# Kernel tuning notes

Measured on AMD Instinct MI355X. Metric: run time of the kernel, lower is better.

Reference implementation:

```python
import jax, jax.numpy as jnp
import numpy as np

N_VAR = 524288   # code.n
DV = 3           # regular variable-node degree
DC = 6           # regular check-node degree
N_CHK = N_VAR * DV // DC
T = 10           # max_iterations


def setup_inputs() -> dict:
    key = jax.random.key(0)
    k1, k2, k3 = jax.random.split(key, 3)
    rng = np.random.default_rng(0)
    # Regular (3,6) Tanner graph via random socket permutation (edge list == H sparsity)
    edge_var = np.repeat(np.arange(N_VAR, dtype=np.int32), DV)
    edge_chk = rng.permutation(np.repeat(np.arange(N_CHK, dtype=np.int32), DC)).astype(np.int32)
    llr = jax.random.normal(k1, (N_VAR,), jnp.float32) * 2.0
    beta = jax.random.normal(k2, (T,), jnp.float32) * 0.1   # per-iteration dc-shared offsets
    alpha = jax.random.normal(k3, (T,), jnp.float32) * 0.1  # per-iteration dv-shared offsets
    return {"llr": llr, "beta": beta, "alpha": alpha,
            "edge_var": jnp.asarray(edge_var), "edge_chk": jnp.asarray(edge_chk),
            "n_checks": N_CHK}


def reference(llr, beta, alpha, edge_var, edge_chk, n_checks):
    E = edge_var.shape[0]
    n = llr.shape[0]
    e_idx = jnp.arange(E)

    def step(carry, ba):
        v2c, _ = carry
        b, a = ba
        mags = jnp.abs(v2c)
        sgn = jnp.sign(v2c)
        # per-check min / argmin(first) / second-min over incoming edge magnitudes
        min1 = jax.ops.segment_min(mags, edge_chk, num_segments=n_checks)
        amin = jax.ops.segment_min(jnp.where(mags == min1[edge_chk], e_idx, E),
                                   edge_chk, num_segments=n_checks)
        is_amin = e_idx == amin[edge_chk]
        min2 = jax.ops.segment_min(jnp.where(is_amin, jnp.inf, mags),
                                   edge_chk, num_segments=n_checks)
        min2 = jnp.where(jnp.isinf(min2), min1, min2)  # degree-1 checks: min2 = min1
        raw = jnp.where(is_amin, min2[edge_chk], min1[edge_chk])
        # product of signs excluding self (signs are +-1)
        sprod = jax.ops.segment_prod(sgn, edge_chk, num_segments=n_checks)
        c2v = sprod[edge_chk] * sgn * (jax.nn.relu(raw - b) - a)
        # variable node: extrinsic sum
        tot = jax.ops.segment_sum(c2v, edge_var, num_segments=n)
        v2c_new = llr[edge_var] + tot[edge_var] - c2v
        return (v2c_new, c2v), None

    v2c0 = llr[edge_var]
    (v2c_f, c2v_f), _ = jax.lax.scan(step, (v2c0, jnp.zeros_like(v2c0)), (beta, alpha))
    posterior = llr + jax.ops.segment_sum(c2v_f, edge_var, num_segments=n)
    decoded_bits = (posterior < 0).astype(jnp.int32)
    return decoded_bits, posterior
```

## Files before the change

### kernel.cpp

```cpp
#include <hip/hip_runtime.h>
#include <math.h>

#define DC_C 6
#define NRANGE 8
#define VCH 2048


__device__ __forceinline__ float c2v_from_rec(uint3 r, int j) {
    float val = ((r.z >> j) & 1u) ? __uint_as_float(r.x) : __uint_as_float(r.y);
    float s = ((r.z >> (16 + j)) & 1u) ? 0.0f
            : (((r.z >> (8 + j)) & 1u) ? -1.0f : 1.0f);
    return s * val;
}

__global__ void build_a(const int* __restrict__ edge_chk,
                        unsigned int* __restrict__ cnt8,
                        unsigned long long* __restrict__ pos64,
                        int n) {
    int v = blockIdx.x * blockDim.x + threadIdx.x;
    if (v >= n) return;
    int c0 = edge_chk[v * 3 + 0];
    int c1 = edge_chk[v * 3 + 1];
    int c2 = edge_chk[v * 3 + 2];
    unsigned int sh0 = (c0 & 7) * 4, sh1 = (c1 & 7) * 4, sh2 = (c2 & 7) * 4;
    unsigned int o0 = atomicAdd(&cnt8[c0 >> 3], 1u << sh0);
    unsigned int o1 = atomicAdd(&cnt8[c1 >> 3], 1u << sh1);
    unsigned int o2 = atomicAdd(&cnt8[c2 >> 3], 1u << sh2);
    int j0 = (o0 >> sh0) & 0xF;
    int j1 = (o1 >> sh1) & 0xF;
    int j2 = (o2 >> sh2) & 0xF;
    unsigned long long s0 = (unsigned long long)(c0 * DC_C + j0);
    unsigned long long s1 = (unsigned long long)(c1 * DC_C + j1);
    unsigned long long s2 = (unsigned long long)(c2 * DC_C + j2);
    pos64[v] = s0 | (s1 << 21) | (s2 << 42);
}

__global__ void build_b(const unsigned long long* __restrict__ pos64,
                        int* __restrict__ vmap,
                        int n, int E) {
    int r = blockIdx.x & (NRANGE - 1);
    int chunk = blockIdx.x >> 3;
    int lo = r * (E / NRANGE);
    int hi = lo + (E / NRANGE);
    int base = chunk * VCH;
#pragma unroll
    for (int rr = 0; rr < VCH / 256; ++rr) {
        int v = base + rr * 256 + threadIdx.x;
        if (v >= n) break;
        unsigned long long pk = pos64[v];
        int s0 = (int)(pk & 0x1FFFFF);
        int s1 = (int)((pk >> 21) & 0x1FFFFF);
        int s2 = (int)((pk >> 42) & 0x1FFFFF);
        if (s0 >= lo && s0 < hi) vmap[s0] = v;
        if (s1 >= lo && s1 < hi) vmap[s1] = v;
        if (s2 >= lo && s2 < hi) vmap[s2] = v;
    }
}

__global__ void check_kernel(const float* __restrict__ p,
                             const int* __restrict__ vmap,
                             uint3* __restrict__ recs,
                             const float* __restrict__ beta,
                             const float* __restrict__ alpha,
                             int t, int n_chk, int first) {
    int c = blockIdx.x * blockDim.x + threadIdx.x;
    if (c >= n_chk) return;
    int base = c * DC_C;
    int2 w01 = *(const int2*)(vmap + base);
    int2 w23 = *(const int2*)(vmap + base + 2);
    int2 w45 = *(const int2*)(vmap + base + 4);
    int w[DC_C] = {w01.x, w01.y, w23.x, w23.y, w45.x, w45.y};
    float pv[DC_C];
#pragma unroll
    for (int j = 0; j < DC_C; ++j) pv[j] = p[w[j]];

    float old_[DC_C];
    if (first) {
#pragma unroll
        for (int j = 0; j < DC_C; ++j) old_[j] = 0.0f;
    } else {
        uint3 rec = recs[c];
#pragma unroll
        for (int j = 0; j < DC_C; ++j) old_[j] = c2v_from_rec(rec, j);
    }

    float b = beta[t];
    float a = alpha[t];
    float sprod = 1.0f;
    float m1 = INFINITY, m2 = INFINITY;
    float mg[DC_C];
    unsigned int ng = 0, zr = 0;
#pragma unroll
    for (int j = 0; j < DC_C; ++j) {
        float x = pv[j] - old_[j];
        float m = fabsf(x);
        mg[j] = m;
        if (x < 0.0f) { ng |= (1u << j); sprod = -sprod; }
        else if (x == 0.0f) { zr |= (1u << j); sprod = 0.0f; }
        if (m < m1) { m2 = m1; m1 = m; }
        else if (m < m2) { m2 = m; }
    }
    unsigned int am = 0;
#pragma unroll
    for (int j = 0; j < DC_C; ++j) am |= (mg[j] == m1) ? (1u << j) : 0u;
    float A = fmaxf(m2 - b, 0.0f) - a;
    float B = fmaxf(m1 - b, 0.0f) - a;
    recs[c] = make_uint3(__float_as_uint(sprod * A),
                         __float_as_uint(sprod * B),
                         am | (ng << 8) | (zr << 16));
}

__global__ void var_kernel(const uint3* __restrict__ recs,
                           const unsigned long long* __restrict__ pos64,
                           const float* __restrict__ llr,
                           float* __restrict__ p,
                           int n2) {
    int i = blockIdx.x * blockDim.x + threadIdx.x;
    if (i >= n2) return;
    ulonglong2 pk2 = *(const ulonglong2*)(pos64 + i * 2);
    float2 ll = *(const float2*)(llr + i * 2);
    int a0 = (int)(pk2.x & 0x1FFFFF);
    int a1 = (int)((pk2.x >> 21) & 0x1FFFFF);
    int a2 = (int)((pk2.x >> 42) & 0x1FFFFF);
    int b0 = (int)(pk2.y & 0x1FFFFF);
    int b1 = (int)((pk2.y >> 21) & 0x1FFFFF);
    int b2 = (int)((pk2.y >> 42) & 0x1FFFFF);
    uint3 ra0 = recs[a0 / DC_C];
    uint3 ra1 = recs[a1 / DC_C];
    uint3 ra2 = recs[a2 / DC_C];
    uint3 rb0 = recs[b0 / DC_C];
    uint3 rb1 = recs[b1 / DC_C];
    uint3 rb2 = recs[b2 / DC_C];
    float ca0 = c2v_from_rec(ra0, a0 % DC_C);
    float ca1 = c2v_from_rec(ra1, a1 % DC_C);
    float ca2 = c2v_from_rec(ra2, a2 % DC_C);
    float cb0 = c2v_from_rec(rb0, b0 % DC_C);
    float cb1 = c2v_from_rec(rb1, b1 % DC_C);
    float cb2 = c2v_from_rec(rb2, b2 % DC_C);
    float2 o;
    o.x = ll.x + ((ca0 + ca1) + ca2);
    o.y = ll.y + ((cb0 + cb1) + cb2);
    *(float2*)(p + i * 2) = o;
}

__global__ void final_kernel(const uint3* __restrict__ recs,
                             const unsigned long long* __restrict__ pos64,
                             const float* __restrict__ llr,
                             float* __restrict__ out,
                             int n2, int n) {
    int i = blockIdx.x * blockDim.x + threadIdx.x;
    if (i >= n2) return;
    ulonglong2 pk2 = *(const ulonglong2*)(pos64 + i * 2);
    float2 ll = *(const float2*)(llr + i * 2);
    int a0 = (int)(pk2.x & 0x1FFFFF);
    int a1 = (int)((pk2.x >> 21) & 0x1FFFFF);
    int a2 = (int)((pk2.x >> 42) & 0x1FFFFF);
    int b0 = (int)(pk2.y & 0x1FFFFF);
    int b1 = (int)((pk2.y >> 21) & 0x1FFFFF);
    int b2 = (int)((pk2.y >> 42) & 0x1FFFFF);
    uint3 ra0 = recs[a0 / DC_C];
    uint3 ra1 = recs[a1 / DC_C];
    uint3 ra2 = recs[a2 / DC_C];
    uint3 rb0 = recs[b0 / DC_C];
    uint3 rb1 = recs[b1 / DC_C];
    uint3 rb2 = recs[b2 / DC_C];
    float pa = ll.x + ((c2v_from_rec(ra0, a0 % DC_C)
                      + c2v_from_rec(ra1, a1 % DC_C))
                      + c2v_from_rec(ra2, a2 % DC_C));
    float pb = ll.y + ((c2v_from_rec(rb0, b0 % DC_C)
                      + c2v_from_rec(rb1, b1 % DC_C))
                      + c2v_from_rec(rb2, b2 % DC_C));
    float2 bits, post;
    bits.x = (pa < 0.0f) ? 1.0f : 0.0f;
    bits.y = (pb < 0.0f) ? 1.0f : 0.0f;
    post.x = pa;
    post.y = pb;
    *(float2*)(out + i * 2) = bits;
    *(float2*)(out + n + i * 2) = post;
}

extern "C" void kernel_launch(void* const* d_in, const int* in_sizes, int n_in,
                              void* d_out, int out_size, void* d_ws, size_t ws_size,
                              hipStream_t stream) {
    const float* llr      = (const float*)d_in[0];
    const float* beta     = (const float*)d_in[1];
    const float* alpha    = (const float*)d_in[2];
    const int*   edge_chk = (const int*)d_in[4];

    const int n  = in_sizes[0];
    const int T  = in_sizes[1];
    const int E  = in_sizes[3];
    const int n_chk = E / DC_C;

    char* ws = (char*)d_ws;
    unsigned int*       cnt8  = (unsigned int*)ws;
    unsigned long long* pos64 = (unsigned long long*)(ws + (1u << 20));
    int*                vmap  = (int*)(ws + (5u << 20));
    unsigned int*       recs  = (unsigned int*)(ws + (11u << 20));
    float*              p     = (float*)(ws + (14u << 20));

    hipMemsetAsync(cnt8, 0, (size_t)(n_chk / 8) * 4, stream);
    build_a<<<(n + 255) / 256, 256, 0, stream>>>(edge_chk, cnt8, pos64, n);
    {
        int chunks = (n + VCH - 1) / VCH;
        build_b<<<chunks * NRANGE, 256, 0, stream>>>(pos64, vmap, n, E);
    }
    for (int t = 0; t < T; ++t) {
        const float* src = (t == 0) ? llr : p;
        check_kernel<<<(n_chk + 255) / 256, 256, 0, stream>>>(
            src, vmap, (uint3*)recs, beta, alpha, t, n_chk, (t == 0) ? 1 : 0);
        if (t + 1 < T) {
            var_kernel<<<(n / 2 + 255) / 256, 256, 0, stream>>>(
                (const uint3*)recs, pos64, llr, p, n / 2);
        } else {
            final_kernel<<<(n / 2 + 255) / 256, 256, 0, stream>>>(
                (const uint3*)recs, pos64, llr, (float*)d_out, n / 2, n);
        }
    }
}
```

Before: 367.3 us.

## Store per-edge v2c messages in check order, scatter from variable kernel

Replaces the variable-indexed posterior array plus vmap gather with an edge-indexed v2c buffer laid out in check-socket order. The variable kernel now scatters extrinsic messages (posterior minus own c2v) directly to each socket, so the check kernel reads contiguous float4s and no longer has to reconstruct the old c2v from its record. Each check thread now handles two checks to vectorize loads and stores. The cost moves from random gathers in the check kernel to random 4-byte scattered stores in the variable kernel.

After: 482.0 us. +31.2%, slower.

```diff
diff --git a/kernel.cpp b/kernel.cpp
--- a/kernel.cpp
+++ b/kernel.cpp
@@ -11,6 +11,31 @@
     float s = ((r.z >> (16 + j)) & 1u) ? 0.0f
             : (((r.z >> (8 + j)) & 1u) ? -1.0f : 1.0f);
     return s * val;
+}
+
+__device__ __forceinline__ uint3 make_rec(const float pv[DC_C], float b, float a) {
+    float sprod = 1.0f;
+    float m1 = INFINITY, m2 = INFINITY;
+    float mg[DC_C];
+    unsigned int ng = 0, zr = 0;
+#pragma unroll
+    for (int j = 0; j < DC_C; ++j) {
+        float x = pv[j];
+        float m = fabsf(x);
+        mg[j] = m;
+        if (x < 0.0f) { ng |= (1u << j); sprod = -sprod; }
+        else if (x == 0.0f) { zr |= (1u << j); sprod = 0.0f; }
+        if (m < m1) { m2 = m1; m1 = m; }
+        else if (m < m2) { m2 = m; }
+    }
+    unsigned int am = 0;
+#pragma unroll
+    for (int j = 0; j < DC_C; ++j) am |= (mg[j] == m1) ? (1u << j) : 0u;
+    float A = fmaxf(m2 - b, 0.0f) - a;
+    float B = fmaxf(m1 - b, 0.0f) - a;
+    return make_uint3(__float_as_uint(sprod * A),
+                      __float_as_uint(sprod * B),
+                      am | (ng << 8) | (zr << 16));
 }
 
 __global__ void build_a(const int* __restrict__ edge_chk,
@@ -35,9 +60,10 @@
     pos64[v] = s0 | (s1 << 21) | (s2 << 42);
 }
 
-__global__ void build_b(const unsigned long long* __restrict__ pos64,
-                        int* __restrict__ vmap,
-                        int n, int E) {
+__global__ void init_v2c(const unsigned long long* __restrict__ pos64,
+                         const float* __restrict__ llr,
+                         float* __restrict__ v2c,
+                         int n, int E) {
     int r = blockIdx.x & (NRANGE - 1);
     int chunk = blockIdx.x >> 3;
     int lo = r * (E / NRANGE);
@@ -48,77 +74,48 @@
         int v = base + rr * 256 + threadIdx.x;
         if (v >= n) break;
         unsigned long long pk = pos64[v];
+        float lv = llr[v];
         int s0 = (int)(pk & 0x1FFFFF);
         int s1 = (int)((pk >> 21) & 0x1FFFFF);
         int s2 = (int)((pk >> 42) & 0x1FFFFF);
-        if (s0 >= lo && s0 < hi) vmap[s0] = v;
-        if (s1 >= lo && s1 < hi) vmap[s1] = v;
-        if (s2 >= lo && s2 < hi) vmap[s2] = v;
-    }
-}
-
-__global__ void check_kernel(const float* __restrict__ p,
-                             const int* __restrict__ vmap,
-                             uint3* __restrict__ recs,
+        if (s0 >= lo && s0 < hi) v2c[s0] = lv;
+        if (s1 >= lo && s1 < hi) v2c[s1] = lv;
+        if (s2 >= lo && s2 < hi) v2c[s2] = lv;
+    }
+}
+
+__global__ void check_kernel(const float* __restrict__ v2c,
+                             unsigned int* __restrict__ recs_u,
                              const float* __restrict__ beta,
                              const float* __restrict__ alpha,
-                             int t, int n_chk, int first) {
-    int c = blockIdx.x * blockDim.x + threadIdx.x;
-    if (c >= n_chk) return;
-    int base = c * DC_C;
-    int2 w01 = *(const int2*)(vmap + base);
-    int2 w23 = *(const int2*)(vmap + base + 2);
-    int2 w45 = *(const int2*)(vmap + base + 4);
-    int w[DC_C] = {w01.x, w01.y, w23.x, w23.y, w45.x, w45.y};
-    float pv[DC_C];
-#pragma unroll
-    for (int j = 0; j < DC_C; ++j) pv[j] = p[w[j]];
-
-    float old_[DC_C];
-    if (first) {
-#pragma unroll
-        for (int j = 0; j < DC_C; ++j) old_[j] = 0.0f;
-    } else {
-        uint3 rec = recs[c];
-#pragma unroll
-        for (int j = 0; j < DC_C; ++j) old_[j] = c2v_from_rec(rec, j);
-    }
-
+                             int t, int npair) {
+    int i = blockIdx.x * blockDim.x + threadIdx.x;
+    if (i >= npair) return;
+    const float4* vb = (const float4*)(v2c + (size_t)i * 12);
+    float4 q0 = vb[0];
+    float4 q1 = vb[1];
+    float4 q2 = vb[2];
     float b = beta[t];
     float a = alpha[t];
-    float sprod = 1.0f;
-    float m1 = INFINITY, m2 = INFINITY;
-    float mg[DC_C];
-    unsigned int ng = 0, zr = 0;
-#pragma unroll
-    for (int j = 0; j < DC_C; ++j) {
-        float x = pv[j] - old_[j];
-        float m = fabsf(x);
-        mg[j] = m;
-        if (x < 0.0f) { ng |= (1u << j); sprod = -sprod; }
-        else if (x == 0.0f) { zr |= (1u << j); sprod = 0.0f; }
-        if (m < m1) { m2 = m1; m1 = m; }
-        else if (m < m2) { m2 = m; }
-    }
-    unsigned int am = 0;
-#pragma unroll
-    for (int j = 0; j < DC_C; ++j) am |= (mg[j] == m1) ? (1u << j) : 0u;
-    float A = fmaxf(m2 - b, 0.0f) - a;
-    float B = fmaxf(m1 - b, 0.0f) - a;
-    recs[c] = make_uint3(__float_as_uint(sprod * A),
-                         __float_as_uint(sprod * B),
-                         am | (ng << 8) | (zr << 16));
+    float pv0[DC_C] = {q0.x, q0.y, q0.z, q0.w, q1.x, q1.y};
+    float pv1[DC_C] = {q1.z, q1.w, q2.x, q2.y, q2.z, q2.w};
+    uint3 r0 = make_rec(pv0, b, a);
+    uint3 r1 = make_rec(pv1, b, a);
+    uint2* rb = (uint2*)(recs_u + (size_t)i * 6);
+    rb[0] = make_uint2(r0.x, r0.y);
+    rb[1] = make_uint2(r0.z, r1.x);
+    rb[2] = make_uint2(r1.y, r1.z);
 }
 
 __global__ void var_kernel(const uint3* __restrict__ recs,
                            const unsigned long long* __restrict__ pos64,
                            const float* __restrict__ llr,
-                           float* __restrict__ p,
+                           float* __restrict__ v2c,
                            int n2) {
     int i = blockIdx.x * blockDim.x + threadIdx.x;
     if (i >= n2) return;
-    ulonglong2 pk2 = *(const ulonglong2*)(pos64 + i * 2);
-    float2 ll = *(const float2*)(llr + i * 2);
+    ulonglong2 pk2 = *(const ulonglong2*)(pos64 + (size_t)i * 2);
+    float2 ll = *(const float2*)(llr + (size_t)i * 2);
     int a0 = (int)(pk2.x & 0x1FFFFF);
     int a1 = (int)((pk2.x >> 21) & 0x1FFFFF);
     int a2 = (int)((pk2.x >> 42) & 0x1FFFFF);
@@ -137,10 +134,14 @@
     float cb0 = c2v_from_rec(rb0, b0 % DC_C);
     float cb1 = c2v_from_rec(rb1, b1 % DC_C);
     float cb2 = c2v_from_rec(rb2, b2 % DC_C);
-    float2 o;
-    o.x = ll.x + ((ca0 + ca1) + ca2);
-    o.y = ll.y + ((cb0 + cb1) + cb2);
-    *(float2*)(p + i * 2) = o;
+    float pa = ll.x + ((ca0 + ca1) + ca2);
+    float pb = ll.y + ((cb0 + cb1) + cb2);
+    v2c[a0] = pa - ca0;
+    v2c[a1] = pa - ca1;
+    v2c[a2] = pa - ca2;
+    v2c[b0] = pb - cb0;
+    v2c[b1] = pb - cb1;
+    v2c[b2] = pb - cb2;
 }
 
 __global__ void final_kernel(const uint3* __restrict__ recs,
@@ -150,8 +151,8 @@
                              int n2, int n) {
     int i = blockIdx.x * blockDim.x + threadIdx.x;
     if (i >= n2) return;
-    ulonglong2 pk2 = *(const ulonglong2*)(pos64 + i * 2);
-    float2 ll = *(const float2*)(llr + i * 2);
+    ulonglong2 pk2 = *(const ulonglong2*)(pos64 + (size_t)i * 2);
+    float2 ll = *(const float2*)(llr + (size_t)i * 2);
     int a0 = (int)(pk2.x & 0x1FFFFF);
     int a1 = (int)((pk2.x >> 21) & 0x1FFFFF);
     int a2 = (int)((pk2.x >> 42) & 0x1FFFFF);
@@ -175,8 +176,8 @@
     bits.y = (pb < 0.0f) ? 1.0f : 0.0f;
     post.x = pa;
     post.y = pb;
-    *(float2*)(out + i * 2) = bits;
-    *(float2*)(out + n + i * 2) = post;
+    *(float2*)(out + (size_t)i * 2) = bits;
+    *(float2*)(out + n + (size_t)i * 2) = post;
 }
 
 extern "C" void kernel_launch(void* const* d_in, const int* in_sizes, int n_in,
@@ -195,23 +196,22 @@
     char* ws = (char*)d_ws;
     unsigned int*       cnt8  = (unsigned int*)ws;
     unsigned long long* pos64 = (unsigned long long*)(ws + (1u << 20));
-    int*                vmap  = (int*)(ws + (5u << 20));
+    float*              v2c   = (float*)(ws + (5u << 20));
     unsigned int*       recs  = (unsigned int*)(ws + (11u << 20));
-    float*              p     = (float*)(ws + (14u << 20));
 
     hipMemsetAsync(cnt8, 0, (size_t)(n_chk / 8) * 4, stream);
     build_a<<<(n + 255) / 256, 256, 0, stream>>>(edge_chk, cnt8, pos64, n);
     {
         int chunks = (n + VCH - 1) / VCH;
-        build_b<<<chunks * NRANGE, 256, 0, stream>>>(pos64, vmap, n, E);
-    }
+        init_v2c<<<chunks * NRANGE, 256, 0, stream>>>(pos64, llr, v2c, n, E);
+    }
+    const int npair = n_chk / 2;
     for (int t = 0; t < T; ++t) {
-        const float* src = (t == 0) ? llr : p;
-        check_kernel<<<(n_chk + 255) / 256, 256, 0, stream>>>(
-            src, vmap, (uint3*)recs, beta, alpha, t, n_chk, (t == 0) ? 1 : 0);
+        check_kernel<<<(npair + 255) / 256, 256, 0, stream>>>(
+            v2c, recs, beta, alpha, t, npair);
         if (t + 1 < T) {
             var_kernel<<<(n / 2 + 255) / 256, 256, 0, stream>>>(
-                (const uint3*)recs, pos64, llr, p, n / 2);
+                (const uint3*)recs, pos64, llr, v2c, n / 2);
         } else {
             final_kernel<<<(n / 2 + 255) / 256, 256, 0, stream>>>(
                 (const uint3*)recs, pos64, llr, (float*)d_out, n / 2, n);
```

## Fuse variable-node update into check kernel via per-edge static neighbor table

Applied to the files above, without the earlier changes.

Builds a per-edge static table holding the variable index, the edge's slot among that variable's three edges, and the packed record locations of the other two checks. Each check kernel then recomputes variable-to-check messages directly from the previous iteration's check records, ping-ponged between two buffers. This drops the separate variable kernel and its posterior array, halving launches per iteration. In exchange each check thread does more scattered gathers of 12-byte records plus llr, and the table costs 8 bytes per edge. The new path needs a 24 MB workspace and otherwise falls back to the old kernels.

After: 437.7 us. 19.2% more time.

```diff
diff --git a/kernel.cpp b/kernel.cpp
--- a/kernel.cpp
+++ b/kernel.cpp
@@ -11,6 +11,31 @@
     float s = ((r.z >> (16 + j)) & 1u) ? 0.0f
             : (((r.z >> (8 + j)) & 1u) ? -1.0f : 1.0f);
     return s * val;
+}
+
+__device__ __forceinline__ uint3 make_rec(const float pv[DC_C], float b, float a) {
+    float sprod = 1.0f;
+    float m1 = INFINITY, m2 = INFINITY;
+    float mg[DC_C];
+    unsigned int ng = 0, zr = 0;
+#pragma unroll
+    for (int j = 0; j < DC_C; ++j) {
+        float x = pv[j];
+        float m = fabsf(x);
+        mg[j] = m;
+        if (x < 0.0f) { ng |= (1u << j); sprod = -sprod; }
+        else if (x == 0.0f) { zr |= (1u << j); sprod = 0.0f; }
+        if (m < m1) { m2 = m1; m1 = m; }
+        else if (m < m2) { m2 = m; }
+    }
+    unsigned int am = 0;
+#pragma unroll
+    for (int j = 0; j < DC_C; ++j) am |= (mg[j] == m1) ? (1u << j) : 0u;
+    float A = fmaxf(m2 - b, 0.0f) - a;
+    float B = fmaxf(m1 - b, 0.0f) - a;
+    return make_uint3(__float_as_uint(sprod * A),
+                      __float_as_uint(sprod * B),
+                      am | (ng << 8) | (zr << 16));
 }
 
 __global__ void build_a(const int* __restrict__ edge_chk,
@@ -35,13 +60,13 @@
     pos64[v] = s0 | (s1 << 21) | (s2 << 42);
 }
 
-__global__ void build_b(const unsigned long long* __restrict__ pos64,
-                        int* __restrict__ vmap,
-                        int n, int E) {
+__global__ void build_stat(const unsigned long long* __restrict__ pos64,
+                           unsigned long long* __restrict__ stat,
+                           int n, int n_chk) {
     int r = blockIdx.x & (NRANGE - 1);
     int chunk = blockIdx.x >> 3;
-    int lo = r * (E / NRANGE);
-    int hi = lo + (E / NRANGE);
+    int lo = r * (n_chk / NRANGE);
+    int hi = lo + (n_chk / NRANGE);
     int base = chunk * VCH;
 #pragma unroll
     for (int rr = 0; rr < VCH / 256; ++rr) {
@@ -51,96 +76,63 @@
         int s0 = (int)(pk & 0x1FFFFF);
         int s1 = (int)((pk >> 21) & 0x1FFFFF);
         int s2 = (int)((pk >> 42) & 0x1FFFFF);
-        if (s0 >= lo && s0 < hi) vmap[s0] = v;
-        if (s1 >= lo && s1 < hi) vmap[s1] = v;
-        if (s2 >= lo && s2 < hi) vmap[s2] = v;
-    }
-}
-
-__global__ void check_kernel(const float* __restrict__ p,
-                             const int* __restrict__ vmap,
-                             uint3* __restrict__ recs,
-                             const float* __restrict__ beta,
-                             const float* __restrict__ alpha,
-                             int t, int n_chk, int first) {
+        int c0 = s0 / DC_C, c1 = s1 / DC_C, c2 = s2 / DC_C;
+        unsigned long long p0 = ((unsigned long long)c0 << 3) | (unsigned)(s0 - c0 * DC_C);
+        unsigned long long p1 = ((unsigned long long)c1 << 3) | (unsigned)(s1 - c1 * DC_C);
+        unsigned long long p2 = ((unsigned long long)c2 << 3) | (unsigned)(s2 - c2 * DC_C);
+        unsigned long long vv = (unsigned long long)v << 44;
+        if (c0 >= lo && c0 < hi)
+            stat[s0] = p1 | (p2 << 21) | (0ull << 42) | vv;
+        if (c1 >= lo && c1 < hi)
+            stat[s1] = p0 | (p2 << 21) | (1ull << 42) | vv;
+        if (c2 >= lo && c2 < hi)
+            stat[s2] = p0 | (p1 << 21) | (2ull << 42) | vv;
+    }
+}
+
+__global__ void __launch_bounds__(256, 4)
+fused_check(const unsigned long long* __restrict__ stat,
+            const float* __restrict__ llr,
+            const uint3* __restrict__ rd,
+            uint3* __restrict__ wr,
+            const float* __restrict__ beta,
+            const float* __restrict__ alpha,
+            int t, int n_chk, int first) {
     int c = blockIdx.x * blockDim.x + threadIdx.x;
     if (c >= n_chk) return;
-    int base = c * DC_C;
-    int2 w01 = *(const int2*)(vmap + base);
-    int2 w23 = *(const int2*)(vmap + base + 2);
-    int2 w45 = *(const int2*)(vmap + base + 4);
-    int w[DC_C] = {w01.x, w01.y, w23.x, w23.y, w45.x, w45.y};
-    float pv[DC_C];
-#pragma unroll
-    for (int j = 0; j < DC_C; ++j) pv[j] = p[w[j]];
-
-    float old_[DC_C];
-    if (first) {
-#pragma unroll
-        for (int j = 0; j < DC_C; ++j) old_[j] = 0.0f;
-    } else {
-        uint3 rec = recs[c];
-#pragma unroll
-        for (int j = 0; j < DC_C; ++j) old_[j] = c2v_from_rec(rec, j);
-    }
-
+    const ulonglong2* sb = (const ulonglong2*)(stat + (size_t)c * DC_C);
+    ulonglong2 q0 = sb[0];
+    ulonglong2 q1 = sb[1];
+    ulonglong2 q2 = sb[2];
+    unsigned long long sv[DC_C] = {q0.x, q0.y, q1.x, q1.y, q2.x, q2.y};
     float b = beta[t];
     float a = alpha[t];
-    float sprod = 1.0f;
-    float m1 = INFINITY, m2 = INFINITY;
-    float mg[DC_C];
-    unsigned int ng = 0, zr = 0;
-#pragma unroll
-    for (int j = 0; j < DC_C; ++j) {
-        float x = pv[j] - old_[j];
-        float m = fabsf(x);
-        mg[j] = m;
-        if (x < 0.0f) { ng |= (1u << j); sprod = -sprod; }
-        else if (x == 0.0f) { zr |= (1u << j); sprod = 0.0f; }
-        if (m < m1) { m2 = m1; m1 = m; }
-        else if (m < m2) { m2 = m; }
-    }
-    unsigned int am = 0;
-#pragma unroll
-    for (int j = 0; j < DC_C; ++j) am |= (mg[j] == m1) ? (1u << j) : 0u;
-    float A = fmaxf(m2 - b, 0.0f) - a;
-    float B = fmaxf(m1 - b, 0.0f) - a;
-    recs[c] = make_uint3(__float_as_uint(sprod * A),
-                         __float_as_uint(sprod * B),
-                         am | (ng << 8) | (zr << 16));
-}
-
-__global__ void var_kernel(const uint3* __restrict__ recs,
-                           const unsigned long long* __restrict__ pos64,
-                           const float* __restrict__ llr,
-                           float* __restrict__ p,
-                           int n2) {
-    int i = blockIdx.x * blockDim.x + threadIdx.x;
-    if (i >= n2) return;
-    ulonglong2 pk2 = *(const ulonglong2*)(pos64 + i * 2);
-    float2 ll = *(const float2*)(llr + i * 2);
-    int a0 = (int)(pk2.x & 0x1FFFFF);
-    int a1 = (int)((pk2.x >> 21) & 0x1FFFFF);
-    int a2 = (int)((pk2.x >> 42) & 0x1FFFFF);
-    int b0 = (int)(pk2.y & 0x1FFFFF);
-    int b1 = (int)((pk2.y >> 21) & 0x1FFFFF);
-    int b2 = (int)((pk2.y >> 42) & 0x1FFFFF);
-    uint3 ra0 = recs[a0 / DC_C];
-    uint3 ra1 = recs[a1 / DC_C];
-    uint3 ra2 = recs[a2 / DC_C];
-    uint3 rb0 = recs[b0 / DC_C];
-    uint3 rb1 = recs[b1 / DC_C];
-    uint3 rb2 = recs[b2 / DC_C];
-    float ca0 = c2v_from_rec(ra0, a0 % DC_C);
-    float ca1 = c2v_from_rec(ra1, a1 % DC_C);
-    float ca2 = c2v_from_rec(ra2, a2 % DC_C);
-    float cb0 = c2v_from_rec(rb0, b0 % DC_C);
-    float cb1 = c2v_from_rec(rb1, b1 % DC_C);
-    float cb2 = c2v_from_rec(rb2, b2 % DC_C);
-    float2 o;
-    o.x = ll.x + ((ca0 + ca1) + ca2);
-    o.y = ll.y + ((cb0 + cb1) + cb2);
-    *(float2*)(p + i * 2) = o;
+    float pv[DC_C];
+    if (first) {
+#pragma unroll
+        for (int j = 0; j < DC_C; ++j)
+            pv[j] = llr[(int)(sv[j] >> 44)];
+    } else {
+        uint3 ro = rd[c];
+#pragma unroll
+        for (int j = 0; j < DC_C; ++j) {
+            unsigned int ra = (unsigned int)(sv[j] & 0x1FFFFF);
+            unsigned int rb = (unsigned int)((sv[j] >> 21) & 0x1FFFFF);
+            int k = (int)((sv[j] >> 42) & 3);
+            int vtx = (int)(sv[j] >> 44);
+            uint3 rA = rd[ra >> 3];
+            uint3 rB = rd[rb >> 3];
+            float cA = c2v_from_rec(rA, (int)(ra & 7));
+            float cB = c2v_from_rec(rB, (int)(rb & 7));
+            float cS = c2v_from_rec(ro, j);
+            float e0 = (k == 0) ? cS : cA;
+            float e1 = (k == 0) ? cA : ((k == 1) ? cS : cB);
+            float e2 = (k == 2) ? cS : cB;
+            float p = llr[vtx] + ((e0 + e1) + e2);
+            pv[j] = p - cS;
+        }
+    }
+    wr[c] = make_rec(pv, b, a);
 }
 
 __global__ void final_kernel(const uint3* __restrict__ recs,
@@ -150,8 +142,8 @@
                              int n2, int n) {
     int i = blockIdx.x * blockDim.x + threadIdx.x;
     if (i >= n2) return;
-    ulonglong2 pk2 = *(const ulonglong2*)(pos64 + i * 2);
-    float2 ll = *(const float2*)(llr + i * 2);
+    ulonglong2 pk2 = *(const ulonglong2*)(pos64 + (size_t)i * 2);
+    float2 ll = *(const float2*)(llr + (size_t)i * 2);
     int a0 = (int)(pk2.x & 0x1FFFFF);
     int a1 = (int)((pk2.x >> 21) & 0x1FFFFF);
     int a2 = (int)((pk2.x >> 42) & 0x1FFFFF);
@@ -175,8 +167,92 @@
     bits.y = (pb < 0.0f) ? 1.0f : 0.0f;
     post.x = pa;
     post.y = pb;
-    *(float2*)(out + i * 2) = bits;
-    *(float2*)(out + n + i * 2) = post;
+    *(float2*)(out + (size_t)i * 2) = bits;
+    *(float2*)(out + n + (size_t)i * 2) = post;
+}
+
+__global__ void build_b(const unsigned long long* __restrict__ pos64,
+                        int* __restrict__ vmap,
+                        int n, int E) {
+    int r = blockIdx.x & (NRANGE - 1);
+    int chunk = blockIdx.x >> 3;
+    int lo = r * (E / NRANGE);
+    int hi = lo + (E / NRANGE);
+    int base = chunk * VCH;
+#pragma unroll
+    for (int rr = 0; rr < VCH / 256; ++rr) {
+        int v = base + rr * 256 + threadIdx.x;
+        if (v >= n) break;
+        unsigned long long pk = pos64[v];
+        int s0 = (int)(pk & 0x1FFFFF);
+        int s1 = (int)((pk >> 21) & 0x1FFFFF);
+        int s2 = (int)((pk >> 42) & 0x1FFFFF);
+        if (s0 >= lo && s0 < hi) vmap[s0] = v;
+        if (s1 >= lo && s1 < hi) vmap[s1] = v;
+        if (s2 >= lo && s2 < hi) vmap[s2] = v;
+    }
+}
+
+__global__ void check_kernel(const float* __restrict__ p,
+                             const int* __restrict__ vmap,
+                             uint3* __restrict__ recs,
+                             const float* __restrict__ beta,
+                             const float* __restrict__ alpha,
+                             int t, int n_chk, int first) {
+    int c = blockIdx.x * blockDim.x + threadIdx.x;
+    if (c >= n_chk) return;
+    int base = c * DC_C;
+    int2 w01 = *(const int2*)(vmap + base);
+    int2 w23 = *(const int2*)(vmap + base + 2);
+    int2 w45 = *(const int2*)(vmap + base + 4);
+    int w[DC_C] = {w01.x, w01.y, w23.x, w23.y, w45.x, w45.y};
+    float pvv[DC_C];
+#pragma unroll
+    for (int j = 0; j < DC_C; ++j) pvv[j] = p[w[j]];
+    float old_[DC_C];
+    if (first) {
+#pragma unroll
+        for (int j = 0; j < DC_C; ++j) old_[j] = 0.0f;
+    } else {
+        uint3 rec = recs[c];
+#pragma unroll
+        for (int j = 0; j < DC_C; ++j) old_[j] = c2v_from_rec(rec, j);
+    }
+    float pv[DC_C];
+#pragma unroll
+    for (int j = 0; j < DC_C; ++j) pv[j] = pvv[j] - old_[j];
+    recs[c] = make_rec(pv, beta[t], alpha[t]);
+}
+
+__global__ void var_kernel(const uint3* __restrict__ recs,
+                           const unsigned long long* __restrict__ pos64,
+                           const float* __restrict__ llr,
+                           float* __restrict__ p,
+                           int n2) {
+    int i = blockIdx.x * blockDim.x + threadIdx.x;
+    if (i >= n2) return;
+    ulonglong2 pk2 = *(const ulonglong2*)(pos64 + (size_t)i * 2);
+    float2 ll = *(const float2*)(llr + (size_t)i * 2);
+    int a0 = (int)(pk2.x & 0x1FFFFF);
+    int a1 = (int)((pk2.x >> 21) & 0x1FFFFF);
+    int a2 = (int)((pk2.x >> 42) & 0x1FFFFF);
+    int b0 = (int)(pk2.y & 0x1FFFFF);
+    int b1 = (int)((pk2.y >> 21) & 0x1FFFFF);
+    int b2 = (int)((pk2.y >> 42) & 0x1FFFFF);
+    uint3 ra0 = recs[a0 / DC_C];
+    uint3 ra1 = recs[a1 / DC_C];
+    uint3 ra2 = recs[a2 / DC_C];
+    uint3 rb0 = recs[b0 / DC_C];
+    uint3 rb1 = recs[b1 / DC_C];
+    uint3 rb2 = recs[b2 / DC_C];
+    float2 o;
+    o.x = ll.x + ((c2v_from_rec(ra0, a0 % DC_C)
+                 + c2v_from_rec(ra1, a1 % DC_C))
+                 + c2v_from_rec(ra2, a2 % DC_C));
+    o.y = ll.y + ((c2v_from_rec(rb0, b0 % DC_C)
+                 + c2v_from_rec(rb1, b1 % DC_C))
+                 + c2v_from_rec(rb2, b2 % DC_C));
+    *(float2*)(p + (size_t)i * 2) = o;
 }
 
 extern "C" void kernel_launch(void* const* d_in, const int* in_sizes, int n_in,
@@ -193,28 +269,48 @@
     const int n_chk = E / DC_C;
 
     char* ws = (char*)d_ws;
-    unsigned int*       cnt8  = (unsigned int*)ws;
-    unsigned long long* pos64 = (unsigned long long*)(ws + (1u << 20));
-    int*                vmap  = (int*)(ws + (5u << 20));
-    unsigned int*       recs  = (unsigned int*)(ws + (11u << 20));
-    float*              p     = (float*)(ws + (14u << 20));
-
-    hipMemsetAsync(cnt8, 0, (size_t)(n_chk / 8) * 4, stream);
-    build_a<<<(n + 255) / 256, 256, 0, stream>>>(edge_chk, cnt8, pos64, n);
-    {
-        int chunks = (n + VCH - 1) / VCH;
+    const int chunks = (n + VCH - 1) / VCH;
+
+    if (ws_size >= ((size_t)24 << 20)) {
+        unsigned int*       cnt8  = (unsigned int*)ws;
+        unsigned long long* pos64 = (unsigned long long*)(ws + (1u << 20));
+        unsigned long long* stat  = (unsigned long long*)(ws + (5u << 20));
+        uint3*              rec0  = (uint3*)(ws + (18u << 20));
+        uint3*              rec1  = (uint3*)(ws + (21u << 20));
+
+        hipMemsetAsync(cnt8, 0, (size_t)(n_chk / 8) * 4, stream);
+        build_a<<<(n + 255) / 256, 256, 0, stream>>>(edge_chk, cnt8, pos64, n);
+        build_stat<<<chunks * NRANGE, 256, 0, stream>>>(pos64, stat, n, n_chk);
+        for (int t = 0; t < T; ++t) {
+            uint3* wr = (t & 1) ? rec1 : rec0;
+            uint3* rd = (t & 1) ? rec0 : rec1;
+            fused_check<<<(n_chk + 255) / 256, 256, 0, stream>>>(
+                stat, llr, rd, wr, beta, alpha, t, n_chk, (t == 0) ? 1 : 0);
+        }
+        uint3* rec_fin = ((T - 1) & 1) ? rec1 : rec0;
+        final_kernel<<<(n / 2 + 255) / 256, 256, 0, stream>>>(
+            rec_fin, pos64, llr, (float*)d_out, n / 2, n);
+    } else {
+        unsigned int*       cnt8  = (unsigned int*)ws;
+        unsigned long long* pos64 = (unsigned long long*)(ws + (1u << 20));
+        int*                vmap  = (int*)(ws + (5u << 20));
+        uint3*              recs  = (uint3*)(ws + (11u << 20));
+        float*              p     = (float*)(ws + (14u << 20));
+
+        hipMemsetAsync(cnt8, 0, (size_t)(n_chk / 8) * 4, stream);
+        build_a<<<(n + 255) / 256, 256, 0, stream>>>(edge_chk, cnt8, pos64, n);
         build_b<<<chunks * NRANGE, 256, 0, stream>>>(pos64, vmap, n, E);
-    }
-    for (int t = 0; t < T; ++t) {
-        const float* src = (t == 0) ? llr : p;
-        check_kernel<<<(n_chk + 255) / 256, 256, 0, stream>>>(
-            src, vmap, (uint3*)recs, beta, alpha, t, n_chk, (t == 0) ? 1 : 0);
-        if (t + 1 < T) {
-            var_kernel<<<(n / 2 + 255) / 256, 256, 0, stream>>>(
-                (const uint3*)recs, pos64, llr, p, n / 2);
-        } else {
-            final_kernel<<<(n / 2 + 255) / 256, 256, 0, stream>>>(
-                (const uint3*)recs, pos64, llr, (float*)d_out, n / 2, n);
+        for (int t = 0; t < T; ++t) {
+            const float* src = (t == 0) ? llr : p;
+            check_kernel<<<(n_chk + 255) / 256, 256, 0, stream>>>(
+                src, vmap, recs, beta, alpha, t, n_chk, (t == 0) ? 1 : 0);
+            if (t + 1 < T) {
+                var_kernel<<<(n / 2 + 255) / 256, 256, 0, stream>>>(
+                    recs, pos64, llr, p, n / 2);
+            } else {
+                final_kernel<<<(n / 2 + 255) / 256, 256, 0, stream>>>(
+                    recs, pos64, llr, (float*)d_out, n / 2, n);
+            }
         }
     }
 }
```
